# Performance work log

Measured on AMD Instinct MI355X. Metric: run time of the kernel, lower is better.

Reference implementation:

```python
import jax, jax.numpy as jnp
import numpy as np

N = 100000      # nodes (patches)
NNZ = 800000    # incidence (node, hyperedge) pairs from H.coo()
E = 16384       # hyperedges
IN = 128        # in_dim == hidden_dim (residual path active)
HID = 128
HEADS = 4
HD = HID // HEADS   # 32, per-head out_dim
QD = 64             # type_query_dim
L = 2               # n_layers
NT = 4              # n_node_types
ET = 3              # n_edge_types


def setup_inputs() -> dict:
    key = jax.random.key(0)
    ks = jax.random.split(key, 12)
    f32 = jnp.float32
    return {
        "x": jax.random.normal(ks[0], (N, IN), f32),
        "node_types": jax.random.randint(ks[1], (N,), 0, NT, jnp.int32),
        "node_idx": jax.random.randint(ks[2], (NNZ,), 0, N, jnp.int32),
        "edge_idx": jax.random.randint(ks[3], (NNZ,), 0, E, jnp.int32),
        "edge_type": jax.random.randint(ks[4], (E,), 0, ET, jnp.int32),
        # per-layer, per-head parameters (leading axes L, HEADS)
        "type_query": (jax.random.normal(ks[5], (L, HEADS, NT, QD), f32) * 0.02),
        "fc1_w": jax.random.normal(ks[6], (L, HEADS, IN + QD, 32), f32) / np.sqrt(IN + QD),
        "fc1_b": jnp.zeros((L, HEADS, 32), f32),
        "fc2_w": jax.random.normal(ks[7], (L, HEADS, 32, 1), f32) / np.sqrt(32.0),
        "fc2_b": jnp.zeros((L, HEADS, 1), f32),
        "Wq": jax.random.normal(ks[8], (L, HEADS, IN, HD), f32) / np.sqrt(IN),
        "Wv": jax.random.normal(ks[9], (L, HEADS, IN, HD), f32) / np.sqrt(IN),
        "edge_ctx": jax.random.normal(ks[10], (L, HEADS, ET, HD), f32) * 0.02,
        "ln_g": jnp.ones((L, HID), f32),
        "ln_b": jnp.zeros((L, HID), f32),
    }


def _seg_softmax(a, seg, num):
    # scatter_softmax over segments `seg` (stable: subtract per-segment max)
    m = jax.ops.segment_max(a, seg, num_segments=num)
    ex = jnp.exp(a - m[seg])
    s = jax.ops.segment_sum(ex, seg, num_segments=num)
    return ex / s[seg]


def _head(h, node_types, node_idx, edge_idx, edge_type, tq, w1, b1, w2, b2, wq, wv, ec):
    # CascadedHyperGAT.forward, one head
    sig = tq[node_types]                                      # (N, QD)
    z = jnp.tanh(jnp.concatenate([h, sig], axis=1) @ w1 + b1)  # (N, 32)
    alpha_type = jax.nn.sigmoid(z @ w2 + b2)[:, 0]             # (N,)
    Q = h @ wq                                                 # (N, HD)
    V = h @ wv                                                 # (N, HD)
    ctx = ec[edge_type][edge_idx]                              # (NNZ, HD)
    a = jnp.sum(Q[node_idx] * ctx, axis=1)                     # (NNZ,)
    a = jnp.where(a >= 0, a, 0.2 * a)                          # leaky_relu(0.2)
    a = a * alpha_type[node_idx]
    attn = _seg_softmax(a, edge_idx, E)                        # (NNZ,)
    edge_feat = jax.ops.segment_sum(attn[:, None] * V[node_idx], edge_idx, num_segments=E)
    node_feat = jax.ops.segment_sum(attn[:, None] * edge_feat[edge_idx], node_idx, num_segments=N)
    return node_feat, edge_feat


def _layernorm(h, g, b, eps=1e-5):
    mu = h.mean(-1, keepdims=True)
    var = ((h - mu) ** 2).mean(-1, keepdims=True)
    return (h - mu) * jax.lax.rsqrt(var + eps) * g + b


def reference(x, node_types, node_idx, edge_idx, edge_type,
              type_query, fc1_w, fc1_b, fc2_w, fc2_b, Wq, Wv, edge_ctx, ln_g, ln_b):
    head_v = jax.vmap(_head, in_axes=(None, None, None, None, None, 0, 0, 0, 0, 0, 0, 0, 0))
    stats = [x]
    h = x
    for l in range(L):  # small static layer count
        nf, _ = head_v(h, node_types, node_idx, edge_idx, edge_type,
                       type_query[l], fc1_w[l], fc1_b[l], fc2_w[l], fc2_b[l],
                       Wq[l], Wv[l], edge_ctx[l])            # (HEADS, N, HD)
        hn = jnp.transpose(nf, (1, 0, 2)).reshape(h.shape[0], -1)  # concat heads -> (N, HID)
        if hn.shape == h.shape:
            hn = hn + h                                       # residual (dims match)
        h = _layernorm(hn, ln_g[l], ln_b[l])
        stats.append(h)
    return jnp.concatenate(stats, axis=-1)                    # (N, IN + HID*L)
```

## Files before the change

### kernel.cpp

```cpp
#include <hip/hip_runtime.h>
#include <math.h>

#define HEADS 4
#define HD 32
#define QD 64
#define DIN 128
#define NTYPES 4
#define ETYPES 3
#define CAP 512
#define WTC 272

typedef __attribute__((ext_vector_type(8))) short bf16x8;
typedef __attribute__((ext_vector_type(4))) float f32x4;
typedef unsigned short ushort_t;

static inline int cdiv(int a, int b){ return (a + b - 1) / b; }

__device__ inline unsigned short f2bf(float f){
  unsigned u = __float_as_uint(f);
  unsigned r = (u + 0x7FFF + ((u >> 16) & 1)) >> 16;
  return (unsigned short)r;
}
__device__ inline float bf2f(unsigned short u){ return __uint_as_float(((unsigned)u) << 16); }

__device__ inline float lgt_get(const ushort_t* __restrict__ lgt, int n, int et, int hh){
  uint2 lg = *(const uint2*)((const char*)lgt + (size_t)n*24 + et*8);
  unsigned u = (hh & 2) ? lg.y : lg.x;
  return bf2f((hh & 1) ? (ushort_t)(u >> 16) : (ushort_t)(u & 0xffff));
}


__global__ __launch_bounds__(256) void hist_k(const int* __restrict__ node_idx,
                                              const int* __restrict__ edge_idx,
                                              int* __restrict__ cnt_e, int* __restrict__ cnt_n,
                                              uint2* __restrict__ ranks, int NNZ)
{
  int i = blockIdx.x*256 + threadIdx.x;
  if (i < NNZ){
    unsigned re = (unsigned)atomicAdd(&cnt_e[edge_idx[i]], 1);
    unsigned rn = (unsigned)atomicAdd(&cnt_n[node_idx[i]], 1);
    uint2 r; r.x = re; r.y = rn;
    ranks[i] = r;
  }
}

__global__ __launch_bounds__(1024) void scan_pass1(const int* __restrict__ in, int* __restrict__ bsums, int n)
{
  __shared__ int sd[1024];
  int i = blockIdx.x*1024 + threadIdx.x;
  sd[threadIdx.x] = (i < n) ? in[i] : 0;
  __syncthreads();
  for (int s = 512; s > 0; s >>= 1){
    if (threadIdx.x < s) sd[threadIdx.x] += sd[threadIdx.x + s];
    __syncthreads();
  }
  if (threadIdx.x == 0) bsums[blockIdx.x] = sd[0];
}

__global__ __launch_bounds__(1024) void scan_pass2(int* __restrict__ bsums, int nb)
{
  __shared__ int sd[1024];
  int v = (threadIdx.x < nb) ? bsums[threadIdx.x] : 0;
  sd[threadIdx.x] = v;
  __syncthreads();
  for (int s = 1; s < 1024; s <<= 1){
    int t = (threadIdx.x >= s) ? sd[threadIdx.x - s] : 0;
    __syncthreads();
    sd[threadIdx.x] += t;
    __syncthreads();
  }
  if (threadIdx.x < nb) bsums[threadIdx.x] = sd[threadIdx.x] - v;
}

__global__ __launch_bounds__(1024) void scan_pass3(const int* __restrict__ in, const int* __restrict__ bsums,
                                                   int* __restrict__ out, int n)
{
  __shared__ int sd[1024];
  int i = blockIdx.x*1024 + threadIdx.x;
  int v = (i < n) ? in[i] : 0;
  sd[threadIdx.x] = v;
  __syncthreads();
  for (int s = 1; s < 1024; s <<= 1){
    int t = (threadIdx.x >= s) ? sd[threadIdx.x - s] : 0;
    __syncthreads();
    sd[threadIdx.x] += t;
    __syncthreads();
  }
  if (i < n) out[i] = bsums[blockIdx.x] + sd[threadIdx.x] - v;
}

__global__ __launch_bounds__(256) void scatter_k(const int* __restrict__ node_idx, const int* __restrict__ edge_idx,
                                                 const uint2* __restrict__ ranks,
                                                 const int* __restrict__ edge_off, const int* __restrict__ node_off,
                                                 uint2* __restrict__ srtE_rec, int NNZ)
{
  int i = blockIdx.x*256 + threadIdx.x;
  if (i >= NNZ) return;
  int n = node_idx[i], e = edge_idx[i];
  uint2 r = ranks[i];
  int pe = edge_off[e] + (int)r.x;
  int pn = node_off[n] + (int)r.y;
  uint2 rec; rec.x = (unsigned)n; rec.y = (unsigned)pn;
  srtE_rec[pe] = rec;
}


__global__ __launch_bounds__(128) void wtprep_k(const float* __restrict__ w1, const float* __restrict__ wv,
                                                short* __restrict__ Wt, int L)
{
  int c = blockIdx.x % 256, l = blockIdx.x / 256;
  int k = threadIdx.x;
  int hh = (c >> 5) & 3, j = c & 31;
  float v;
  if (c < 128) v = w1[((((size_t)l*HEADS + hh)*(DIN+QD)) + k)*32 + j];
  else         v = wv[((((size_t)l*HEADS + hh)*DIN) + k)*32 + j];
  Wt[((size_t)l*WTC + c)*128 + k] = (short)f2bf(v);
}

__global__ __launch_bounds__(128) void wqc_k(const float* __restrict__ wq, const float* __restrict__ ec,
                                             short* __restrict__ Wt)
{
  int b = blockIdx.x;
  int l = b / 12, c = b % 12, h = c / 3, et = c % 3;
  int k = threadIdx.x;
  const float* wrow = wq + ((((size_t)l*HEADS + h)*DIN) + k)*32;
  const float* ecp  = ec + (((size_t)l*HEADS + h)*ETYPES + et)*32;
  float s = 0.f;
  #pragma unroll
  for (int d = 0; d < 32; d++) s += wrow[d] * ecp[d];
  Wt[((size_t)l*WTC + 256 + c)*128 + k] = (short)f2bf(s);
}

__global__ __launch_bounds__(32) void sbias_k(const float* __restrict__ tq, const float* __restrict__ w1,
                                              const float* __restrict__ b1, float* __restrict__ sbias)
{
  int b = blockIdx.x;
  int ty = b % NTYPES; int hh = (b / NTYPES) % HEADS; int l = b / (NTYPES*HEADS);
  int j = threadIdx.x;
  const float* tqp = tq + (((size_t)l*HEADS + hh)*NTYPES + ty)*QD;
  const float* w1p = w1 + ((size_t)l*HEADS + hh)*(DIN+QD)*32;
  float s = b1[((size_t)l*HEADS + hh)*32 + j];
  for (int k = 0; k < QD; k++) s += tqp[k] * w1p[(size_t)(DIN + k)*32 + j];
  sbias[(size_t)b*32 + j] = s;
}


__device__ inline void load_afrag(const float* __restrict__ h, int hstride, int N,
                                  int rbase, int mf, int l15, int l4, int kk, bf16x8& a)
{
  int row = rbase + mf*16 + l15;
  int rr = (row < N) ? row : (N-1);
  const float* pa = h + (size_t)rr*hstride + kk*32 + l4*8;
  float4 f0 = *(const float4*)pa;
  float4 f1 = *(const float4*)(pa + 4);
  a[0] = (short)f2bf(f0.x); a[1] = (short)f2bf(f0.y);
  a[2] = (short)f2bf(f0.z); a[3] = (short)f2bf(f0.w);
  a[4] = (short)f2bf(f1.x); a[5] = (short)f2bf(f1.y);
  a[6] = (short)f2bf(f1.z); a[7] = (short)f2bf(f1.w);
}


__global__ __launch_bounds__(256) void gemma_k(
    const float* __restrict__ h, int hstride,
    const short* __restrict__ Wt,
    const int* __restrict__ node_types,
    const float* __restrict__ sbias,
    const float* __restrict__ w2,
    const float* __restrict__ b2,
    ushort_t* __restrict__ lgt,
    int N)
{
  __shared__ float alds[128][HEADS];
  int lane = threadIdx.x & 63, wvid = threadIdx.x >> 6;
  int wr = wvid >> 1, wc = wvid & 1;
  int l15 = lane & 15, l4 = lane >> 4;
  int rbase = blockIdx.x*128 + wr*64;

  f32x4 acc[4][4] = {};
  f32x4 acc_e[4] = {};

  #pragma unroll
  for (int kk = 0; kk < 4; kk++){
    bf16x8 a[4], b[4];
    #pragma unroll
    for (int mf = 0; mf < 4; mf++) load_afrag(h, hstride, N, rbase, mf, l15, l4, kk, a[mf]);
    #pragma unroll
    for (int cf = 0; cf < 4; cf++){
      int col = wc*64 + cf*16 + l15;
      b[cf] = *(const bf16x8*)(Wt + (size_t)col*128 + kk*32 + l4*8);
    }
    #pragma unroll
    for (int mf = 0; mf < 4; mf++)
      #pragma unroll
      for (int cf = 0; cf < 4; cf++)
        acc[mf][cf] = __builtin_amdgcn_mfma_f32_16x16x32_bf16(a[mf], b[cf], acc[mf][cf], 0, 0, 0);
    if (wc == 0){
      int ecol = 256 + ((l15 < 12) ? l15 : 11);
      bf16x8 be = *(const bf16x8*)(Wt + (size_t)ecol*128 + kk*32 + l4*8);
      #pragma unroll
      for (int mf = 0; mf < 4; mf++)
        acc_e[mf] = __builtin_amdgcn_mfma_f32_16x16x32_bf16(a[mf], be, acc_e[mf], 0, 0, 0);
    }
  }

  #pragma unroll
  for (int mf = 0; mf < 4; mf++){
    int rw[4], ty[4];
    #pragma unroll
    for (int r = 0; r < 4; r++){
      rw[r] = rbase + mf*16 + l4*4 + r;
      ty[r] = (rw[r] < N) ? node_types[rw[r]] : 0;
    }
    #pragma unroll
    for (int p = 0; p < 2; p++){
      int hh = wc*2 + p;
      float w2a = w2[hh*32 + l15];
      float w2b = w2[hh*32 + 16 + l15];
      float b2v = b2[hh];
      #pragma unroll
      for (int r = 0; r < 4; r++){
        const float* sb = sbias + ((size_t)hh*NTYPES + ty[r])*32;
        float z0 = acc[mf][2*p  ][r] + sb[l15];
        float z1 = acc[mf][2*p+1][r] + sb[16 + l15];
        float t0 = 1.f - 2.f/(__expf(2.f*z0) + 1.f);
        float t1 = 1.f - 2.f/(__expf(2.f*z1) + 1.f);
        float val = t0*w2a + t1*w2b;
        val += __shfl_xor(val, 1); val += __shfl_xor(val, 2);
        val += __shfl_xor(val, 4); val += __shfl_xor(val, 8);
        if (l15 == 0)
          alds[wr*64 + mf*16 + l4*4 + r][hh] = 1.f/(1.f + __expf(-(val + b2v)));
      }
    }
  }
  __syncthreads();

  if (wc == 0 && l15 < 12){
    int hq = l15 / 3, et = l15 % 3;
    #pragma unroll
    for (int mf = 0; mf < 4; mf++){
      #pragma unroll
      for (int r = 0; r < 4; r++){
        int rowloc = wr*64 + mf*16 + l4*4 + r;
        int row = blockIdx.x*128 + rowloc;
        if (row < N){
          float s = acc_e[mf][r] * alds[rowloc][hq];
          s = (s >= 0.f) ? s : 0.2f*s;
          lgt[(size_t)row*12 + et*4 + hq] = f2bf(s);
        }
      }
    }
  }
}


__global__ __launch_bounds__(256) void gemmv_k(
    const float* __restrict__ h, int hstride,
    const short* __restrict__ Wt,
    ushort_t* __restrict__ vb,
    int N)
{
  int lane = threadIdx.x & 63, wvid = threadIdx.x >> 6;
  int wr = wvid >> 1, wc = wvid & 1;
  int l15 = lane & 15, l4 = lane >> 4;
  int rbase = blockIdx.x*128 + wr*64;

  f32x4 acc[4][4] = {};

  #pragma unroll
  for (int kk = 0; kk < 4; kk++){
    bf16x8 a[4], b[4];
    #pragma unroll
    for (int mf = 0; mf < 4; mf++) load_afrag(h, hstride, N, rbase, mf, l15, l4, kk, a[mf]);
    #pragma unroll
    for (int cf = 0; cf < 4; cf++){
      int col = 128 + wc*64 + cf*16 + l15;
      b[cf] = *(const bf16x8*)(Wt + (size_t)col*128 + kk*32 + l4*8);
    }
    #pragma unroll
    for (int mf = 0; mf < 4; mf++)
      #pragma unroll
      for (int cf = 0; cf < 4; cf++)
        acc[mf][cf] = __builtin_amdgcn_mfma_f32_16x16x32_bf16(a[mf], b[cf], acc[mf][cf], 0, 0, 0);
  }

  #pragma unroll
  for (int mf = 0; mf < 4; mf++){
    #pragma unroll
    for (int r = 0; r < 4; r++){
      int row = rbase + mf*16 + l4*4 + r;
      if (row < N){
        #pragma unroll
        for (int cf = 0; cf < 4; cf++){
          int c = wc*64 + cf*16 + l15;
          int hh = c >> 5, d = c & 31;
          vb[((size_t)hh*N + row)*32 + d] = f2bf(acc[mf][cf][r]);
        }
      }
    }
  }
}


__global__ __launch_bounds__(256) void k2b_f(
    const ushort_t* __restrict__ lgt, const ushort_t* __restrict__ vb,
    const uint2* __restrict__ srtE_rec, const int* __restrict__ edge_off, const int* __restrict__ cnt_e,
    const int* __restrict__ edge_type,
    ushort_t* __restrict__ efb,
    uint4* __restrict__ attn_rec,
    int N, int E)
{
  __shared__ float lbuf[HEADS][CAP];
  __shared__ int   nbuf[CAP];
  __shared__ int   pnbuf[CAP];
  __shared__ float mi[HEADS][2];

  int e = blockIdx.x;
  int off = edge_off[e], cnt = cnt_e[e];
  if (cnt == 0) return;
  int lane = threadIdx.x & 63, hh = threadIdx.x >> 6;
  int g = lane & 15, grp = lane >> 4;
  int et = edge_type[e];

  if (cnt <= CAP){
    float mloc = -INFINITY;
    for (int j = lane; j < cnt; j += 64){
      uint2 rc = srtE_rec[off + j];
      float s = lgt_get(lgt, (int)rc.x, et, hh);
      lbuf[hh][j] = s;
      if (hh == 0){ nbuf[j] = (int)rc.x; pnbuf[j] = (int)rc.y; }
      mloc = fmaxf(mloc, s);
    }
    #pragma unroll
    for (int sh = 32; sh > 0; sh >>= 1) mloc = fmaxf(mloc, __shfl_xor(mloc, sh));
    float m = mloc;
    __syncthreads();

    float ef0 = 0.f, ef1 = 0.f, ssum = 0.f;
    const int cm1 = cnt - 1;
    const ushort_t* vbh = vb + (size_t)hh*N*32;
    for (int jj = 0; jj < cnt; jj += 16){
      int j0 = jj + grp, j1 = j0 + 4, j2 = j0 + 8, j3 = j0 + 12;
      int n0 = nbuf[(j0 < cm1) ? j0 : cm1];
      int n1 = nbuf[(j1 < cm1) ? j1 : cm1];
      int n2 = nbuf[(j2 < cm1) ? j2 : cm1];
      int n3 = nbuf[(j3 < cm1) ? j3 : cm1];
      unsigned w0 = *(const unsigned*)&vbh[(size_t)n0*32 + 2*g];
      unsigned w1 = *(const unsigned*)&vbh[(size_t)n1*32 + 2*g];
      unsigned w2 = *(const unsigned*)&vbh[(size_t)n2*32 + 2*g];
      unsigned w3 = *(const unsigned*)&vbh[(size_t)n3*32 + 2*g];
      float e0 = (j0 < cnt) ? __expf(lbuf[hh][j0] - m) : 0.f;
      float e1 = (j1 < cnt) ? __expf(lbuf[hh][j1] - m) : 0.f;
      float e2 = (j2 < cnt) ? __expf(lbuf[hh][j2] - m) : 0.f;
      float e3 = (j3 < cnt) ? __expf(lbuf[hh][j3] - m) : 0.f;
      ef0 += e0*bf2f((ushort_t)(w0 & 0xffff)) + e1*bf2f((ushort_t)(w1 & 0xffff))
           + e2*bf2f((ushort_t)(w2 & 0xffff)) + e3*bf2f((ushort_t)(w3 & 0xffff));
      ef1 += e0*bf2f((ushort_t)(w0 >> 16)) + e1*bf2f((ushort_t)(w1 >> 16))
           + e2*bf2f((ushort_t)(w2 >> 16)) + e3*bf2f((ushort_t)(w3 >> 16));
      ssum += e0 + e1 + e2 + e3;
    }
    ef0 += __shfl_xor(ef0, 16); ef0 += __shfl_xor(ef0, 32);
    ef1 += __shfl_xor(ef1, 16); ef1 += __shfl_xor(ef1, 32);
    ssum += __shfl_xor(ssum, 16); ssum += __shfl_xor(ssum, 32);
    float inv = 1.0f / ssum;
    if (grp == 0){
      unsigned w = (unsigned)f2bf(ef0*inv) | ((unsigned)f2bf(ef1*inv) << 16);
      *(unsigned*)&efb[(size_t)e*128 + hh*32 + 2*g] = w;
    }
    if (lane == 0){ mi[hh][0] = m; mi[hh][1] = inv; }
    __syncthreads();

    if (hh == 0){
      for (int j = lane; j < cnt; j += 64){
        int pn = pnbuf[j];
        float a0 = __expf(lbuf[0][j] - mi[0][0]) * mi[0][1];
        float a1 = __expf(lbuf[1][j] - mi[1][0]) * mi[1][1];
        float a2 = __expf(lbuf[2][j] - mi[2][0]) * mi[2][1];
        float a3 = __expf(lbuf[3][j] - mi[3][0]) * mi[3][1];
        uint4 o;
        o.x = (unsigned)e;
        o.y = (unsigned)f2bf(a0) | ((unsigned)f2bf(a1) << 16);
        o.z = (unsigned)f2bf(a2) | ((unsigned)f2bf(a3) << 16);
        o.w = 0u;
        attn_rec[pn] = o;
      }
    }
  } else {
    float mloc = -INFINITY;
    for (int j = lane; j < cnt; j += 64)
      mloc = fmaxf(mloc, lgt_get(lgt, (int)srtE_rec[off + j].x, et, hh));
    #pragma unroll
    for (int sh = 32; sh > 0; sh >>= 1) mloc = fmaxf(mloc, __shfl_xor(mloc, sh));
    float m = mloc;

    float ef0 = 0.f, ef1 = 0.f, ssum = 0.f;
    for (int jj = 0; jj < cnt; jj += 4){
      int j = jj + grp;
      if (j < cnt){
        int n = (int)srtE_rec[off + j].x;
        float ex = __expf(lgt_get(lgt, n, et, hh) - m);
        unsigned vw = *(const unsigned*)&vb[((size_t)hh*N + n)*32 + 2*g];
        ef0 += ex * bf2f((unsigned short)(vw & 0xffff));
        ef1 += ex * bf2f((unsigned short)(vw >> 16));
        ssum += ex;
      }
    }
    ef0 += __shfl_xor(ef0, 16); ef0 += __shfl_xor(ef0, 32);
    ef1 += __shfl_xor(ef1, 16); ef1 += __shfl_xor(ef1, 32);
    ssum += __shfl_xor(ssum, 16); ssum += __shfl_xor(ssum, 32);
    float inv = 1.0f / ssum;
    if (grp == 0){
      unsigned w = (unsigned)f2bf(ef0*inv) | ((unsigned)f2bf(ef1*inv) << 16);
      *(unsigned*)&efb[(size_t)e*128 + hh*32 + 2*g] = w;
    }
    for (int j = lane; j < cnt; j += 64){
      uint2 rc = srtE_rec[off + j];
      float ex = __expf(lgt_get(lgt, (int)rc.x, et, hh) - m);
      ushort_t* p = (ushort_t*)&attn_rec[rc.y];
      p[2 + hh] = f2bf(ex * inv);
      if (hh == 0){
        ((unsigned*)p)[0] = (unsigned)e;
        ((unsigned*)p)[3] = 0u;
      }
    }
  }
}


__global__ __launch_bounds__(256) void k2c(
    const uint4* __restrict__ attn_rec,
    const int* __restrict__ node_off, const int* __restrict__ cnt_n,
    const ushort_t* __restrict__ efb,
    const float* __restrict__ h_in, int hstride,
    const float* __restrict__ ln_g, const float* __restrict__ ln_b,
    float* __restrict__ out, int out_stride, int out_col, int N, int E)
{
  int wv = threadIdx.x >> 6, lane = threadIdx.x & 63;
  int n = blockIdx.x*4 + wv;
  if (n >= N) return;
  int off = node_off[n], cnt = cnt_n[n];
  int hh = lane >> 4;
  float nf0 = 0.f, nf1 = 0.f;

  for (int j0 = 0; j0 < cnt; j0 += 8){
    int mm = cnt - j0; if (mm > 8) mm = 8;
    uint4 rc = make_uint4(0u, 0u, 0u, 0u);
    if (lane < mm) rc = attn_rec[off + j0 + lane];
    unsigned w[8]; float av[8];
    #pragma unroll
    for (int j = 0; j < 8; j++){
      unsigned ej = (unsigned)__shfl((int)rc.x, j);
      unsigned ay = (unsigned)__shfl((int)rc.y, j);
      unsigned az = (unsigned)__shfl((int)rc.z, j);
      unsigned u = (hh & 2) ? az : ay;
      float a = bf2f((hh & 1) ? (ushort_t)(u >> 16) : (ushort_t)(u & 0xffff));
      av[j] = (j < mm) ? a : 0.f;
      w[j] = *(const unsigned*)&efb[(size_t)ej*128 + 2*lane];
    }
    #pragma unroll
    for (int j = 0; j < 8; j++){
      nf0 += av[j] * bf2f((ushort_t)(w[j] & 0xffff));
      nf1 += av[j] * bf2f((ushort_t)(w[j] >> 16));
    }
  }

  float2 hr = *(const float2*)&h_in[(size_t)n*hstride + 2*lane];
  float hn0 = nf0 + hr.x, hn1 = nf1 + hr.y;

  float s = hn0 + hn1;
  #pragma unroll
  for (int sh = 32; sh > 0; sh >>= 1) s += __shfl_xor(s, sh);
  float mu = s * (1.0f/128.0f);
  float d0 = hn0 - mu, d1 = hn1 - mu;
  float s2 = d0*d0 + d1*d1;
  #pragma unroll
  for (int sh = 32; sh > 0; sh >>= 1) s2 += __shfl_xor(s2, sh);
  float r = rsqrtf(s2*(1.0f/128.0f) + 1e-5f);

  float2 g2 = *(const float2*)&ln_g[2*lane];
  float2 b2 = *(const float2*)&ln_b[2*lane];
  float2 o2;
  o2.x = d0*r*g2.x + b2.x;
  o2.y = d1*r*g2.y + b2.y;
  *(float2*)&out[(size_t)n*out_stride + out_col + 2*lane] = o2;
}


__global__ __launch_bounds__(256) void xcopy_k(const float* __restrict__ x, float* __restrict__ out, int N)
{
  int i = blockIdx.x*256 + threadIdx.x;
  if (i >= N*32) return;
  int n = i >> 5, k = i & 31;
  reinterpret_cast<float4*>(out)[(size_t)n*96 + k] = reinterpret_cast<const float4*>(x)[i];
}


extern "C" void kernel_launch(void* const* d_in, const int* in_sizes, int n_in,
                              void* d_out, int out_size, void* d_ws, size_t ws_size,
                              hipStream_t stream)
{
  const float* x          = (const float*)d_in[0];
  const int*   node_types = (const int*)  d_in[1];
  const int*   node_idx   = (const int*)  d_in[2];
  const int*   edge_idx   = (const int*)  d_in[3];
  const int*   edge_type  = (const int*)  d_in[4];
  const float* type_query = (const float*)d_in[5];
  const float* fc1_w      = (const float*)d_in[6];
  const float* fc1_b      = (const float*)d_in[7];
  const float* fc2_w      = (const float*)d_in[8];
  const float* fc2_b      = (const float*)d_in[9];
  const float* Wq         = (const float*)d_in[10];
  const float* Wv         = (const float*)d_in[11];
  const float* edge_ctx   = (const float*)d_in[12];
  const float* ln_g       = (const float*)d_in[13];
  const float* ln_b       = (const float*)d_in[14];

  const int N   = in_sizes[1];
  const int NNZ = in_sizes[2];
  const int E   = in_sizes[4];
  const int L   = 2;

  char* ws = (char*)d_ws;
  size_t o = 0;
  auto alloc = [&](size_t bytes)->void*{
    void* p = ws + o;
    o = (o + bytes + 255) & ~(size_t)255;
    return p;
  };
  int* cnt_e     = (int*)alloc((size_t)E*4);
  int* edge_off  = (int*)alloc((size_t)(E+1)*4);
  int* cnt_n     = (int*)alloc((size_t)N*4);
  int* node_off  = (int*)alloc((size_t)(N+1)*4);
  uint2* ranks   = (uint2*)alloc((size_t)NNZ*8);
  uint2* srtE_rec= (uint2*)alloc((size_t)NNZ*8);
  int* bsum      = (int*)alloc((size_t)1024*4);
  uint4* attn_rec = (uint4*)alloc((size_t)NNZ*16);
  ushort_t* vb      = (ushort_t*)alloc((size_t)HEADS*N*32*2);
  ushort_t* lgt     = (ushort_t*)alloc((size_t)N*12*2);
  ushort_t* efb     = (ushort_t*)alloc((size_t)E*128*2);
  short*    Wt      = (short*)alloc((size_t)L*WTC*128*2);
  float*    sbias   = (float*)alloc((size_t)L*HEADS*NTYPES*32*4);
  if (o > ws_size) return;

  hipMemsetAsync(cnt_e, 0, (size_t)E*4, stream);
  hipMemsetAsync(cnt_n, 0, (size_t)N*4, stream);

  hist_k<<<cdiv(NNZ,256),256,0,stream>>>(node_idx, edge_idx, cnt_e, cnt_n, ranks, NNZ);

  int nbE = cdiv(E,1024), nbN = cdiv(N,1024);
  scan_pass1<<<nbE,1024,0,stream>>>(cnt_e, bsum, E);
  scan_pass2<<<1,1024,0,stream>>>(bsum, nbE);
  scan_pass3<<<nbE,1024,0,stream>>>(cnt_e, bsum, edge_off, E);
  scan_pass1<<<nbN,1024,0,stream>>>(cnt_n, bsum, N);
  scan_pass2<<<1,1024,0,stream>>>(bsum, nbN);
  scan_pass3<<<nbN,1024,0,stream>>>(cnt_n, bsum, node_off, N);

  scatter_k<<<cdiv(NNZ,256),256,0,stream>>>(node_idx, edge_idx, ranks, edge_off, node_off,
                                            srtE_rec, NNZ);

  wtprep_k<<<L*256,128,0,stream>>>(fc1_w, Wv, Wt, L);
  wqc_k<<<L*12,128,0,stream>>>(Wq, edge_ctx, Wt);
  sbias_k<<<L*HEADS*NTYPES,32,0,stream>>>(type_query, fc1_w, fc1_b, sbias);

  xcopy_k<<<cdiv(N*32,256),256,0,stream>>>(x, (float*)d_out, N);

  for (int l = 0; l < L; l++){
    const float* hin = (l == 0) ? x : ((const float*)d_out + 128);
    int hstride = (l == 0) ? DIN : (3*DIN);

    gemma_k<<<cdiv(N,128),256,0,stream>>>(
        hin, hstride,
        Wt + (size_t)l*WTC*128,
        node_types,
        sbias + (size_t)l*HEADS*NTYPES*32,
        fc2_w + (size_t)l*HEADS*32,
        fc2_b + (size_t)l*HEADS,
        lgt, N);

    gemmv_k<<<cdiv(N,128),256,0,stream>>>(
        hin, hstride,
        Wt + (size_t)l*WTC*128,
        vb, N);

    k2b_f<<<E,256,0,stream>>>(lgt, vb, srtE_rec, edge_off, cnt_e,
                              edge_type, efb, attn_rec, N, E);

    k2c<<<cdiv(N,4),256,0,stream>>>(attn_rec, node_off, cnt_n, efb,
                                    hin, hstride,
                                    ln_g + (size_t)l*DIN, ln_b + (size_t)l*DIN,
                                    (float*)d_out, 3*DIN, DIN + l*DIN, N, E);
  }
}
```

Before: 549.9 us.

## Fuse attention and value GEMMs, merge edge/node scans, fold x-copy into LN kernel

```diff
diff --git a/kernel.cpp b/kernel.cpp
--- a/kernel.cpp
+++ b/kernel.cpp
@@ -32,13 +32,13 @@
 
 __global__ __launch_bounds__(256) void hist_k(const int* __restrict__ node_idx,
                                               const int* __restrict__ edge_idx,
-                                              int* __restrict__ cnt_e, int* __restrict__ cnt_n,
-                                              uint2* __restrict__ ranks, int NNZ)
+                                              int* __restrict__ cnt,
+                                              uint2* __restrict__ ranks, int E, int NNZ)
 {
   int i = blockIdx.x*256 + threadIdx.x;
   if (i < NNZ){
-    unsigned re = (unsigned)atomicAdd(&cnt_e[edge_idx[i]], 1);
-    unsigned rn = (unsigned)atomicAdd(&cnt_n[node_idx[i]], 1);
+    unsigned re = (unsigned)atomicAdd(&cnt[edge_idx[i]], 1);
+    unsigned rn = (unsigned)atomicAdd(&cnt[E + node_idx[i]], 1);
     uint2 r; r.x = re; r.y = rn;
     ranks[i] = r;
   }
@@ -91,15 +91,15 @@
 
 __global__ __launch_bounds__(256) void scatter_k(const int* __restrict__ node_idx, const int* __restrict__ edge_idx,
                                                  const uint2* __restrict__ ranks,
-                                                 const int* __restrict__ edge_off, const int* __restrict__ node_off,
-                                                 uint2* __restrict__ srtE_rec, int NNZ)
+                                                 const int* __restrict__ off,
+                                                 uint2* __restrict__ srtE_rec, int E, int NNZ)
 {
   int i = blockIdx.x*256 + threadIdx.x;
   if (i >= NNZ) return;
   int n = node_idx[i], e = edge_idx[i];
   uint2 r = ranks[i];
-  int pe = edge_off[e] + (int)r.x;
-  int pn = node_off[n] + (int)r.y;
+  int pe = off[e] + (int)r.x;
+  int pn = off[E + n] - NNZ + (int)r.y;
   uint2 rec; rec.x = (unsigned)n; rec.y = (unsigned)pn;
   srtE_rec[pe] = rec;
 }
@@ -160,7 +160,7 @@
 }
 
 
-__global__ __launch_bounds__(256) void gemma_k(
+__global__ __launch_bounds__(256) void gemm_f2(
     const float* __restrict__ h, int hstride,
     const short* __restrict__ Wt,
     const int* __restrict__ node_types,
@@ -168,13 +168,14 @@
     const float* __restrict__ w2,
     const float* __restrict__ b2,
     ushort_t* __restrict__ lgt,
+    ushort_t* __restrict__ vb,
     int N)
 {
-  __shared__ float alds[128][HEADS];
+  __shared__ float alds[64][HEADS];
   int lane = threadIdx.x & 63, wvid = threadIdx.x >> 6;
-  int wr = wvid >> 1, wc = wvid & 1;
   int l15 = lane & 15, l4 = lane >> 4;
-  int rbase = blockIdx.x*128 + wr*64;
+  int rbase = blockIdx.x*64;
+  int wtcol0 = (wvid < 2) ? wvid*64 : (128 + (wvid - 2)*64);
 
   f32x4 acc[4][4] = {};
   f32x4 acc_e[4] = {};
@@ -186,7 +187,7 @@
     for (int mf = 0; mf < 4; mf++) load_afrag(h, hstride, N, rbase, mf, l15, l4, kk, a[mf]);
     #pragma unroll
     for (int cf = 0; cf < 4; cf++){
-      int col = wc*64 + cf*16 + l15;
+      int col = wtcol0 + cf*16 + l15;
       b[cf] = *(const bf16x8*)(Wt + (size_t)col*128 + kk*32 + l4*8);
     }
     #pragma unroll
@@ -194,7 +195,7 @@
       #pragma unroll
       for (int cf = 0; cf < 4; cf++)
         acc[mf][cf] = __builtin_amdgcn_mfma_f32_16x16x32_bf16(a[mf], b[cf], acc[mf][cf], 0, 0, 0);
-    if (wc == 0){
+    if (wvid == 0){
       int ecol = 256 + ((l15 < 12) ? l15 : 11);
       bf16x8 be = *(const bf16x8*)(Wt + (size_t)ecol*128 + kk*32 + l4*8);
       #pragma unroll
@@ -203,97 +204,67 @@
     }
   }
 
-  #pragma unroll
-  for (int mf = 0; mf < 4; mf++){
-    int rw[4], ty[4];
-    #pragma unroll
-    for (int r = 0; r < 4; r++){
-      rw[r] = rbase + mf*16 + l4*4 + r;
-      ty[r] = (rw[r] < N) ? node_types[rw[r]] : 0;
-    }
-    #pragma unroll
-    for (int p = 0; p < 2; p++){
-      int hh = wc*2 + p;
-      float w2a = w2[hh*32 + l15];
-      float w2b = w2[hh*32 + 16 + l15];
-      float b2v = b2[hh];
+  if (wvid < 2){
+    #pragma unroll
+    for (int mf = 0; mf < 4; mf++){
+      int rw[4], ty[4];
       #pragma unroll
       for (int r = 0; r < 4; r++){
-        const float* sb = sbias + ((size_t)hh*NTYPES + ty[r])*32;
-        float z0 = acc[mf][2*p  ][r] + sb[l15];
-        float z1 = acc[mf][2*p+1][r] + sb[16 + l15];
-        float t0 = 1.f - 2.f/(__expf(2.f*z0) + 1.f);
-        float t1 = 1.f - 2.f/(__expf(2.f*z1) + 1.f);
-        float val = t0*w2a + t1*w2b;
-        val += __shfl_xor(val, 1); val += __shfl_xor(val, 2);
-        val += __shfl_xor(val, 4); val += __shfl_xor(val, 8);
-        if (l15 == 0)
-          alds[wr*64 + mf*16 + l4*4 + r][hh] = 1.f/(1.f + __expf(-(val + b2v)));
-      }
-    }
-  }
-  __syncthreads();
-
-  if (wc == 0 && l15 < 12){
-    int hq = l15 / 3, et = l15 % 3;
+        rw[r] = rbase + mf*16 + l4*4 + r;
+        ty[r] = (rw[r] < N) ? node_types[rw[r]] : 0;
+      }
+      #pragma unroll
+      for (int p = 0; p < 2; p++){
+        int hh = wvid*2 + p;
+        float w2a = w2[hh*32 + l15];
+        float w2b = w2[hh*32 + 16 + l15];
+        float b2v = b2[hh];
+        #pragma unroll
+        for (int r = 0; r < 4; r++){
+          const float* sb = sbias + ((size_t)hh*NTYPES + ty[r])*32;
+          float z0 = acc[mf][2*p  ][r] + sb[l15];
+          float z1 = acc[mf][2*p+1][r] + sb[16 + l15];
+          float t0 = 1.f - 2.f/(__expf(2.f*z0) + 1.f);
+          float t1 = 1.f - 2.f/(__expf(2.f*z1) + 1.f);
+          float val = t0*w2a + t1*w2b;
+          val += __shfl_xor(val, 1); val += __shfl_xor(val, 2);
+          val += __shfl_xor(val, 4); val += __shfl_xor(val, 8);
+          if (l15 == 0)
+            alds[mf*16 + l4*4 + r][hh] = 1.f/(1.f + __expf(-(val + b2v)));
+        }
+      }
+    }
+  } else {
     #pragma unroll
     for (int mf = 0; mf < 4; mf++){
       #pragma unroll
       for (int r = 0; r < 4; r++){
-        int rowloc = wr*64 + mf*16 + l4*4 + r;
-        int row = blockIdx.x*128 + rowloc;
+        int row = rbase + mf*16 + l4*4 + r;
+        if (row < N){
+          #pragma unroll
+          for (int cf = 0; cf < 4; cf++){
+            int c = (wvid - 2)*64 + cf*16 + l15;
+            int hh = c >> 5, d = c & 31;
+            vb[((size_t)hh*N + row)*32 + d] = f2bf(acc[mf][cf][r]);
+          }
+        }
+      }
+    }
+  }
+  __syncthreads();
+
+  if (wvid == 0 && l15 < 12){
+    int hq = l15 / 3, et = l15 % 3;
+    #pragma unroll
+    for (int mf = 0; mf < 4; mf++){
+      #pragma unroll
+      for (int r = 0; r < 4; r++){
+        int rowloc = mf*16 + l4*4 + r;
+        int row = rbase + rowloc;
         if (row < N){
           float s = acc_e[mf][r] * alds[rowloc][hq];
           s = (s >= 0.f) ? s : 0.2f*s;
           lgt[(size_t)row*12 + et*4 + hq] = f2bf(s);
-        }
-      }
-    }
-  }
-}
-
-
-__global__ __launch_bounds__(256) void gemmv_k(
-    const float* __restrict__ h, int hstride,
-    const short* __restrict__ Wt,
-    ushort_t* __restrict__ vb,
-    int N)
-{
-  int lane = threadIdx.x & 63, wvid = threadIdx.x >> 6;
-  int wr = wvid >> 1, wc = wvid & 1;
-  int l15 = lane & 15, l4 = lane >> 4;
-  int rbase = blockIdx.x*128 + wr*64;
-
-  f32x4 acc[4][4] = {};
-
-  #pragma unroll
-  for (int kk = 0; kk < 4; kk++){
-    bf16x8 a[4], b[4];
-    #pragma unroll
-    for (int mf = 0; mf < 4; mf++) load_afrag(h, hstride, N, rbase, mf, l15, l4, kk, a[mf]);
-    #pragma unroll
-    for (int cf = 0; cf < 4; cf++){
-      int col = 128 + wc*64 + cf*16 + l15;
-      b[cf] = *(const bf16x8*)(Wt + (size_t)col*128 + kk*32 + l4*8);
-    }
-    #pragma unroll
-    for (int mf = 0; mf < 4; mf++)
-      #pragma unroll
-      for (int cf = 0; cf < 4; cf++)
-        acc[mf][cf] = __builtin_amdgcn_mfma_f32_16x16x32_bf16(a[mf], b[cf], acc[mf][cf], 0, 0, 0);
-  }
-
-  #pragma unroll
-  for (int mf = 0; mf < 4; mf++){
-    #pragma unroll
-    for (int r = 0; r < 4; r++){
-      int row = rbase + mf*16 + l4*4 + r;
-      if (row < N){
-        #pragma unroll
-        for (int cf = 0; cf < 4; cf++){
-          int c = wc*64 + cf*16 + l15;
-          int hh = c >> 5, d = c & 31;
-          vb[((size_t)hh*N + row)*32 + d] = f2bf(acc[mf][cf][r]);
         }
       }
     }
@@ -322,18 +293,23 @@
   int et = edge_type[e];
 
   if (cnt <= CAP){
+    for (int j = threadIdx.x; j < cnt; j += 256){
+      uint2 rc = srtE_rec[off + j];
+      uint2 lg = *(const uint2*)((const char*)lgt + (size_t)rc.x*24 + et*8);
+      lbuf[0][j] = bf2f((ushort_t)(lg.x & 0xffff));
+      lbuf[1][j] = bf2f((ushort_t)(lg.x >> 16));
+      lbuf[2][j] = bf2f((ushort_t)(lg.y & 0xffff));
+      lbuf[3][j] = bf2f((ushort_t)(lg.y >> 16));
+      nbuf[j] = (int)rc.x;
+      pnbuf[j] = (int)rc.y;
+    }
+    __syncthreads();
+
     float mloc = -INFINITY;
-    for (int j = lane; j < cnt; j += 64){
-      uint2 rc = srtE_rec[off + j];
-      float s = lgt_get(lgt, (int)rc.x, et, hh);
-      lbuf[hh][j] = s;
-      if (hh == 0){ nbuf[j] = (int)rc.x; pnbuf[j] = (int)rc.y; }
-      mloc = fmaxf(mloc, s);
-    }
+    for (int j = lane; j < cnt; j += 64) mloc = fmaxf(mloc, lbuf[hh][j]);
     #pragma unroll
     for (int sh = 32; sh > 0; sh >>= 1) mloc = fmaxf(mloc, __shfl_xor(mloc, sh));
     float m = mloc;
-    __syncthreads();
 
     float ef0 = 0.f, ef1 = 0.f, ssum = 0.f;
     const int cm1 = cnt - 1;
@@ -428,16 +404,16 @@
 
 __global__ __launch_bounds__(256) void k2c(
     const uint4* __restrict__ attn_rec,
-    const int* __restrict__ node_off, const int* __restrict__ cnt_n,
+    const int* __restrict__ node_off, const int* __restrict__ cnt_n, int noff_shift,
     const ushort_t* __restrict__ efb,
     const float* __restrict__ h_in, int hstride,
     const float* __restrict__ ln_g, const float* __restrict__ ln_b,
-    float* __restrict__ out, int out_stride, int out_col, int N, int E)
+    float* __restrict__ out, int out_stride, int out_col, int do_xcopy, int N, int E)
 {
   int wv = threadIdx.x >> 6, lane = threadIdx.x & 63;
   int n = blockIdx.x*4 + wv;
   if (n >= N) return;
-  int off = node_off[n], cnt = cnt_n[n];
+  int off = node_off[n] - noff_shift, cnt = cnt_n[n];
   int hh = lane >> 4;
   float nf0 = 0.f, nf1 = 0.f;
 
@@ -464,6 +440,8 @@
   }
 
   float2 hr = *(const float2*)&h_in[(size_t)n*hstride + 2*lane];
+  if (do_xcopy)
+    *(float2*)&out[(size_t)n*out_stride + 2*lane] = hr;
   float hn0 = nf0 + hr.x, hn1 = nf1 + hr.y;
 
   float s = hn0 + hn1;
@@ -482,15 +460,6 @@
   o2.x = d0*r*g2.x + b2.x;
   o2.y = d1*r*g2.y + b2.y;
   *(float2*)&out[(size_t)n*out_stride + out_col + 2*lane] = o2;
-}
-
-
-__global__ __launch_bounds__(256) void xcopy_k(const float* __restrict__ x, float* __restrict__ out, int N)
-{
-  int i = blockIdx.x*256 + threadIdx.x;
-  if (i >= N*32) return;
-  int n = i >> 5, k = i & 31;
-  reinterpret_cast<float4*>(out)[(size_t)n*96 + k] = reinterpret_cast<const float4*>(x)[i];
 }
 
 
@@ -518,6 +487,7 @@
   const int NNZ = in_sizes[2];
   const int E   = in_sizes[4];
   const int L   = 2;
+  const int EN  = E + N;
 
   char* ws = (char*)d_ws;
   size_t o = 0;
@@ -526,10 +496,8 @@
     o = (o + bytes + 255) & ~(size_t)255;
     return p;
   };
-  int* cnt_e     = (int*)alloc((size_t)E*4);
-  int* edge_off  = (int*)alloc((size_t)(E+1)*4);
-  int* cnt_n     = (int*)alloc((size_t)N*4);
-  int* node_off  = (int*)alloc((size_t)(N+1)*4);
+  int* cnt       = (int*)alloc((size_t)EN*4);
+  int* off       = (int*)alloc((size_t)(EN+1)*4);
   uint2* ranks   = (uint2*)alloc((size_t)NNZ*8);
   uint2* srtE_rec= (uint2*)alloc((size_t)NNZ*8);
   int* bsum      = (int*)alloc((size_t)1024*4);
@@ -541,52 +509,40 @@
   float*    sbias   = (float*)alloc((size_t)L*HEADS*NTYPES*32*4);
   if (o > ws_size) return;
 
-  hipMemsetAsync(cnt_e, 0, (size_t)E*4, stream);
-  hipMemsetAsync(cnt_n, 0, (size_t)N*4, stream);
-
-  hist_k<<<cdiv(NNZ,256),256,0,stream>>>(node_idx, edge_idx, cnt_e, cnt_n, ranks, NNZ);
-
-  int nbE = cdiv(E,1024), nbN = cdiv(N,1024);
-  scan_pass1<<<nbE,1024,0,stream>>>(cnt_e, bsum, E);
-  scan_pass2<<<1,1024,0,stream>>>(bsum, nbE);
-  scan_pass3<<<nbE,1024,0,stream>>>(cnt_e, bsum, edge_off, E);
-  scan_pass1<<<nbN,1024,0,stream>>>(cnt_n, bsum, N);
-  scan_pass2<<<1,1024,0,stream>>>(bsum, nbN);
-  scan_pass3<<<nbN,1024,0,stream>>>(cnt_n, bsum, node_off, N);
-
-  scatter_k<<<cdiv(NNZ,256),256,0,stream>>>(node_idx, edge_idx, ranks, edge_off, node_off,
-                                            srtE_rec, NNZ);
+  hipMemsetAsync(cnt, 0, (size_t)EN*4, stream);
+
+  hist_k<<<cdiv(NNZ,256),256,0,stream>>>(node_idx, edge_idx, cnt, ranks, E, NNZ);
+
+  int nb = cdiv(EN,1024);
+  scan_pass1<<<nb,1024,0,stream>>>(cnt, bsum, EN);
+  scan_pass2<<<1,1024,0,stream>>>(bsum, nb);
+  scan_pass3<<<nb,1024,0,stream>>>(cnt, bsum, off, EN);
+
+  scatter_k<<<cdiv(NNZ,256),256,0,stream>>>(node_idx, edge_idx, ranks, off, srtE_rec, E, NNZ);
 
   wtprep_k<<<L*256,128,0,stream>>>(fc1_w, Wv, Wt, L);
   wqc_k<<<L*12,128,0,stream>>>(Wq, edge_ctx, Wt);
   sbias_k<<<L*HEADS*NTYPES,32,0,stream>>>(type_query, fc1_w, fc1_b, sbias);
 
-  xcopy_k<<<cdiv(N*32,256),256,0,stream>>>(x, (float*)d_out, N);
-
   for (int l = 0; l < L; l++){
     const float* hin = (l == 0) ? x : ((const float*)d_out + 128);
     int hstride = (l == 0) ? DIN : (3*DIN);
 
-    gemma_k<<<cdiv(N,128),256,0,stream>>>(
+    gemm_f2<<<cdiv(N,64),256,0,stream>>>(
         hin, hstride,
         Wt + (size_t)l*WTC*128,
         node_types,
         sbias + (size_t)l*HEADS*NTYPES*32,
         fc2_w + (size_t)l*HEADS*32,
         fc2_b + (size_t)l*HEADS,
-        lgt, N);
-
-    gemmv_k<<<cdiv(N,128),256,0,stream>>>(
-        hin, hstride,
-        Wt + (size_t)l*WTC*128,
-        vb, N);
-
-    k2b_f<<<E,256,0,stream>>>(lgt, vb, srtE_rec, edge_off, cnt_e,
+        lgt, vb, N);
+
+    k2b_f<<<E,256,0,stream>>>(lgt, vb, srtE_rec, off, cnt,
                               edge_type, efb, attn_rec, N, E);
 
-    k2c<<<cdiv(N,4),256,0,stream>>>(attn_rec, node_off, cnt_n, efb,
+    k2c<<<cdiv(N,4),256,0,stream>>>(attn_rec, off + E, cnt + E, NNZ, efb,
                                     hin, hstride,
                                     ln_g + (size_t)l*DIN, ln_b + (size_t)l*DIN,
-                                    (float*)d_out, 3*DIN, DIN + l*DIN, N, E);
-  }
-}
+                                    (float*)d_out, 3*DIN, DIN + l*DIN, (l == 0) ? 1 : 0, N, E);
+  }
+}
```

Measured after the change: 554.8 us. About the same (+0.9%).
